# Kernel tuning notes

Hardware: AMD Instinct MI355X
Metric: run time of the kernel (lower is better)

## Reference

```python
import jax, jax.numpy as jnp
import numpy as np

NUM_HEADS = 12
MASK_BIAS = -1000.0


def setup_inputs() -> dict:
    key = jax.random.key(0)
    k1, k2, k3, k4 = jax.random.split(key, 4)
    B, N, C = 2, 2048, 768
    x = jax.random.normal(k1, (B, N, C), dtype=jnp.float32)
    # key-padding mask: 1.0 = masked-out position (gets -1000 bias), 0.0 = visible
    mask = jax.random.randint(k2, (B, N), 0, 2).astype(jnp.float32)
    qkv_w = jax.random.normal(k3, (3 * C, C), dtype=jnp.float32) * (1.0 / np.sqrt(C))
    proj_w = jax.random.normal(k4, (C, C), dtype=jnp.float32) * (1.0 / np.sqrt(C))
    proj_b = jnp.zeros((C,), dtype=jnp.float32)
    return {"x": x, "mask": mask, "qkv_w": qkv_w, "proj_w": proj_w, "proj_b": proj_b}


def reference(x, mask, qkv_w, proj_w, proj_b):
    B, N, C = x.shape
    H = NUM_HEADS
    D = C // H
    scale = D ** (-0.5)
    # qkv: Linear without bias -> [B, N, 3C] -> [3, B, H, N, D]
    qkv = (x @ qkv_w.T).reshape(B, N, 3, H, D).transpose(2, 0, 3, 1, 4)
    q, k, v = qkv[0], qkv[1], qkv[2]
    # scores [B, H, N, N]
    attn = jnp.einsum("bhqd,bhkd->bhqk", q, k) * scale
    attn = attn + mask[:, None, None, :] * MASK_BIAS
    attn = jax.nn.softmax(attn, axis=-1)
    out = jnp.einsum("bhqk,bhkd->bhqd", attn, v)  # [B, H, N, D]
    out = out.transpose(0, 2, 1, 3).reshape(B, N, C)
    return out @ proj_w.T + proj_b
```

## Files before the change

### kernel.cpp

```cpp
#include <hip/hip_runtime.h>

typedef __bf16 bf16_t;
typedef __bf16 bf16x8 __attribute__((ext_vector_type(8)));
typedef float f32x4 __attribute__((ext_vector_type(4)));

#define NUM_B 2
#define NUM_H 12
#define SEQ_N 2048
#define DIM_C 768
#define HEAD_D 64
#define BH_CNT (NUM_B * NUM_H)
#define MTOK (NUM_B * SEQ_N)
#define QSCALE 0.1803368801111137f

#define AS1(p) ((const __attribute__((address_space(1))) void*)(p))
#define AS3(p) ((__attribute__((address_space(3))) void*)(p))

__global__ __launch_bounds__(256) void cvt_scan_kernel(
    const float* __restrict__ s0, const float* __restrict__ s1,
    const float* __restrict__ s2, const float* __restrict__ msk,
    bf16_t* __restrict__ d0, bf16_t* __restrict__ d1, bf16_t* __restrict__ d2,
    int* __restrict__ src, bf16_t* __restrict__ wp, int* __restrict__ cnts,
    int nb0, int nb1, int nb2) {
  __shared__ int psum[256];
  const int blk = blockIdx.x;
  const int t = threadIdx.x;
  if (blk >= nb0 + nb1 + nb2) {
    const int b = blk - (nb0 + nb1 + nb2);
    const float* mb = msk + (size_t)b * SEQ_N;
    int vis[8], c = 0;
#pragma unroll
    for (int j = 0; j < 8; ++j) {
      vis[j] = (mb[t * 8 + j] == 0.0f) ? 1 : 0;
      c += vis[j];
    }
    psum[t] = c;
    __syncthreads();
    for (int off = 1; off < 256; off <<= 1) {
      int v = (t >= off) ? psum[t - off] : 0;
      __syncthreads();
      psum[t] += v;
      __syncthreads();
    }
    const int total = psum[255];
    int vpos = psum[t] - c;
    int mpos = total + (t * 8 - (psum[t] - c));
#pragma unroll
    for (int j = 0; j < 8; ++j) {
      const int tok = t * 8 + j;
      if (vis[j]) {
        src[b * SEQ_N + vpos] = b * SEQ_N + tok;
        wp[b * SEQ_N + vpos] = (bf16_t)1.0f;
        ++vpos;
      } else {
        src[b * SEQ_N + mpos] = b * SEQ_N + tok;
        wp[b * SEQ_N + mpos] = (bf16_t)0.0f;
        ++mpos;
      }
    }
    if (t == 0) {
      cnts[b * 2] = (total + 63) & ~63;
      cnts[b * 2 + 1] = total;
    }
    return;
  }
  const float* sp;
  bf16_t* dp;
  size_t off;
  if (blk < nb0) {
    sp = s0; dp = d0; off = (size_t)blk * 2048;
  } else if (blk < nb0 + nb1) {
    sp = s1; dp = d1; off = (size_t)(blk - nb0) * 2048;
  } else {
    sp = s2; dp = d2; off = (size_t)(blk - nb0 - nb1) * 2048;
  }
  const size_t i = off + (size_t)t * 8;
  float4 f0 = *reinterpret_cast<const float4*>(&sp[i]);
  float4 f1 = *reinterpret_cast<const float4*>(&sp[i + 4]);
  union { ushort4 u; bf16_t h[4]; } p0, p1;
  p0.h[0] = (bf16_t)f0.x; p0.h[1] = (bf16_t)f0.y;
  p0.h[2] = (bf16_t)f0.z; p0.h[3] = (bf16_t)f0.w;
  p1.h[0] = (bf16_t)f1.x; p1.h[1] = (bf16_t)f1.y;
  p1.h[2] = (bf16_t)f1.z; p1.h[3] = (bf16_t)f1.w;
  *reinterpret_cast<ushort4*>(&dp[i]) = p0.u;
  *reinterpret_cast<ushort4*>(&dp[i + 4]) = p1.u;
}

__global__ __launch_bounds__(256, 3) void gemm_qkv_kernel(
    const bf16_t* __restrict__ A, const bf16_t* __restrict__ W,
    const int* __restrict__ src, const int* __restrict__ cnts,
    bf16_t* __restrict__ out) {
  __shared__ __align__(16) bf16_t As[2][128 * 32];
  __shared__ __align__(16) bf16_t Bs[2][128 * 32];

  const int tid = threadIdx.x;
  const int wave = tid >> 6, lane = tid & 63;
  const int quad = lane >> 4, l16 = lane & 15;
  const int m0 = blockIdx.y * 128, n0 = blockIdx.x * 128;
  const int wm = (wave >> 1) * 64, wn = (wave & 1) * 64;
  const bool isQ = (n0 < DIM_C);

  if (!isQ) {
    const int b = m0 >> 11;
    if ((m0 & 2047) >= cnts[b * 2]) return;
  }

  f32x4 acc[4][4] = {};

  const int srow = tid >> 2;
  const int scol = ((tid & 3) ^ ((tid >> 3) & 3)) * 8;
  int ar0, ar1;
  if (isQ) {
    ar0 = m0 + srow;
    ar1 = m0 + srow + 64;
  } else {
    ar0 = src[m0 + srow];
    ar1 = src[m0 + srow + 64];
  }
  const bf16_t* gA0 = A + (size_t)ar0 * DIM_C + scol;
  const bf16_t* gA1 = A + (size_t)ar1 * DIM_C + scol;
  const bf16_t* gB0 = W + (size_t)(n0 + srow) * DIM_C + scol;
  const bf16_t* gB1 = W + (size_t)(n0 + srow + 64) * DIM_C + scol;
  const int lb = wave * 512;

  auto issue = [&](int buf, int k0) {
    __builtin_amdgcn_global_load_lds(AS1(gA0 + k0), AS3(&As[buf][lb]), 16, 0, 0);
    __builtin_amdgcn_global_load_lds(AS1(gA1 + k0), AS3(&As[buf][lb + 2048]), 16, 0, 0);
    __builtin_amdgcn_global_load_lds(AS1(gB0 + k0), AS3(&Bs[buf][lb]), 16, 0, 0);
    __builtin_amdgcn_global_load_lds(AS1(gB1 + k0), AS3(&Bs[buf][lb + 2048]), 16, 0, 0);
  };

  issue(0, 0);
  int cur = 0;
  const int sw = (l16 >> 1) & 3;
  for (int step = 0; step < DIM_C / 32; ++step) {
    __syncthreads();
    if (step + 1 < DIM_C / 32) issue(cur ^ 1, (step + 1) * 32);

    bf16x8 aF[4], bF[4];
#pragma unroll
    for (int mi = 0; mi < 4; ++mi)
      aF[mi] = *reinterpret_cast<const bf16x8*>(
          &As[cur][(wm + mi * 16 + l16) * 32 + ((quad ^ sw) * 8)]);
#pragma unroll
    for (int ni = 0; ni < 4; ++ni)
      bF[ni] = *reinterpret_cast<const bf16x8*>(
          &Bs[cur][(wn + ni * 16 + l16) * 32 + ((quad ^ sw) * 8)]);
#pragma unroll
    for (int mi = 0; mi < 4; ++mi)
#pragma unroll
      for (int ni = 0; ni < 4; ++ni)
        acc[mi][ni] = __builtin_amdgcn_mfma_f32_16x16x32_bf16(aF[mi], bF[ni],
                                                              acc[mi][ni], 0, 0, 0);
    cur ^= 1;
  }

  const size_t per = (size_t)BH_CNT * SEQ_N * HEAD_D;
#pragma unroll
  for (int mi = 0; mi < 4; ++mi) {
#pragma unroll
    for (int ni = 0; ni < 4; ++ni) {
      const int gmB = m0 + wm + mi * 16 + quad * 4;
      const int gn = n0 + wn + ni * 16 + l16;
      const int b = gmB >> 11;
      if (isQ) {
        const int h = gn >> 6, d = gn & 63;
#pragma unroll
        for (int r = 0; r < 4; ++r) {
          const int gm = gmB + r;
          const int tok = gm & 2047;
          out[(((size_t)((gm >> 11) * NUM_H + h) * SEQ_N + tok) * HEAD_D + d)] =
              (bf16_t)(acc[mi][ni][r] * QSCALE);
        }
      } else if (n0 < 2 * DIM_C) {
        const int rem = gn - DIM_C;
        const int h = rem >> 6, d = rem & 63;
#pragma unroll
        for (int r = 0; r < 4; ++r) {
          const int pos = (gmB + r) & 2047;
          out[per + (((size_t)(b * NUM_H + h) * SEQ_N + pos) * HEAD_D + d)] =
              (bf16_t)acc[mi][ni][r];
        }
      } else {
        const int rem = gn - 2 * DIM_C;
        const int h = rem >> 6, d = rem & 63;
        const int pos0 = gmB & 2047;
        const int count = cnts[b * 2 + 1];
        union { ushort4 u; bf16_t h4[4]; } pk;
#pragma unroll
        for (int r = 0; r < 4; ++r)
          pk.h4[r] = (pos0 + r < count) ? (bf16_t)acc[mi][ni][r] : (bf16_t)0.0f;
        *reinterpret_cast<ushort4*>(
            &out[2 * per + (((size_t)(b * NUM_H + h) * HEAD_D + d) * SEQ_N + pos0)]) =
            pk.u;
      }
    }
  }
}

__global__ __launch_bounds__(256, 3) void gemm_proj_kernel(
    const bf16_t* __restrict__ A, const bf16_t* __restrict__ W,
    const float* __restrict__ bias, float* __restrict__ out) {
  __shared__ __align__(16) bf16_t As[2][128 * 32];
  __shared__ __align__(16) bf16_t Bs[2][128 * 32];

  const int tid = threadIdx.x;
  const int wave = tid >> 6, lane = tid & 63;
  const int quad = lane >> 4, l16 = lane & 15;
  const int m0 = blockIdx.y * 128, n0 = blockIdx.x * 128;
  const int wm = (wave >> 1) * 64, wn = (wave & 1) * 64;

  f32x4 acc[4][4] = {};

  const int srow = tid >> 2;
  const int scol = ((tid & 3) ^ ((tid >> 3) & 3)) * 8;
  const bf16_t* gA0 = A + (size_t)(m0 + srow) * DIM_C + scol;
  const bf16_t* gA1 = A + (size_t)(m0 + srow + 64) * DIM_C + scol;
  const bf16_t* gB0 = W + (size_t)(n0 + srow) * DIM_C + scol;
  const bf16_t* gB1 = W + (size_t)(n0 + srow + 64) * DIM_C + scol;
  const int lb = wave * 512;

  auto issue = [&](int buf, int k0) {
    __builtin_amdgcn_global_load_lds(AS1(gA0 + k0), AS3(&As[buf][lb]), 16, 0, 0);
    __builtin_amdgcn_global_load_lds(AS1(gA1 + k0), AS3(&As[buf][lb + 2048]), 16, 0, 0);
    __builtin_amdgcn_global_load_lds(AS1(gB0 + k0), AS3(&Bs[buf][lb]), 16, 0, 0);
    __builtin_amdgcn_global_load_lds(AS1(gB1 + k0), AS3(&Bs[buf][lb + 2048]), 16, 0, 0);
  };

  issue(0, 0);
  int cur = 0;
  const int sw = (l16 >> 1) & 3;
  for (int step = 0; step < DIM_C / 32; ++step) {
    __syncthreads();
    if (step + 1 < DIM_C / 32) issue(cur ^ 1, (step + 1) * 32);

    bf16x8 aF[4], bF[4];
#pragma unroll
    for (int mi = 0; mi < 4; ++mi)
      aF[mi] = *reinterpret_cast<const bf16x8*>(
          &As[cur][(wm + mi * 16 + l16) * 32 + ((quad ^ sw) * 8)]);
#pragma unroll
    for (int ni = 0; ni < 4; ++ni)
      bF[ni] = *reinterpret_cast<const bf16x8*>(
          &Bs[cur][(wn + ni * 16 + l16) * 32 + ((quad ^ sw) * 8)]);
#pragma unroll
    for (int mi = 0; mi < 4; ++mi)
#pragma unroll
      for (int ni = 0; ni < 4; ++ni)
        acc[mi][ni] = __builtin_amdgcn_mfma_f32_16x16x32_bf16(aF[mi], bF[ni],
                                                              acc[mi][ni], 0, 0, 0);
    cur ^= 1;
  }

#pragma unroll
  for (int mi = 0; mi < 4; ++mi) {
#pragma unroll
    for (int ni = 0; ni < 4; ++ni) {
      const int gmB = m0 + wm + mi * 16 + quad * 4;
      const int gn = n0 + wn + ni * 16 + l16;
      const float bv = bias[gn];
#pragma unroll
      for (int r = 0; r < 4; ++r)
        out[(size_t)(gmB + r) * DIM_C + gn] = acc[mi][ni][r] + bv;
    }
  }
}

__global__ __launch_bounds__(256, 3) void attn_kernel(
    const bf16_t* __restrict__ q, const bf16_t* __restrict__ k,
    const bf16_t* __restrict__ vt, const bf16_t* __restrict__ wp,
    const int* __restrict__ cnts, bf16_t* __restrict__ ctx) {
  __shared__ __align__(16) bf16_t Ks[2][128 * 64];
  __shared__ __align__(16) bf16_t Ps[4][1024];

  const int tid = threadIdx.x;
  const int wave = tid >> 6, lane = tid & 63;
  const int quad = lane >> 4, l16 = lane & 15;
  const int bh = blockIdx.y;
  const int b = bh / NUM_H, h = bh - b * NUM_H;
  const int q0 = blockIdx.x * 64 + wave * 16;
  const int cntPad = cnts[b * 2];

  const bf16_t* qb = q + (size_t)bh * SEQ_N * HEAD_D;
  const bf16_t* kb = k + (size_t)bh * SEQ_N * HEAD_D;
  const bf16_t* vtb = vt + (size_t)bh * HEAD_D * SEQ_N;
  const bf16_t* wb = wp + (size_t)b * SEQ_N;

  bf16x8 qf[2];
#pragma unroll
  for (int ks = 0; ks < 2; ++ks)
    qf[ks] = *reinterpret_cast<const bf16x8*>(
        &qb[(size_t)(q0 + l16) * HEAD_D + ks * 32 + quad * 8]);

  f32x4 acc[4] = {};
  f32x4 acc_l = {};

  const int srow = tid >> 3;
  const int scol = ((tid & 7) ^ (srow & 7)) * 8;
  const bf16_t* gK = kb + (size_t)srow * HEAD_D + scol;
  const int lb = wave * 512;

  auto issueK = [&](int buf, int key0) {
#pragma unroll
    for (int p = 0; p < 4; ++p)
      __builtin_amdgcn_global_load_lds(
          AS1(gK + (size_t)(key0 + p * 32) * HEAD_D),
          AS3(&Ks[buf][p * 2048 + lb]), 16, 0, 0);
  };

  issueK(0, 0);
  int cur = 0;
  const int swz = l16 & 7;
  const int psbase = wave * 1024 + l16 * 64;

  for (int key0 = 0; key0 < cntPad; key0 += 128) {
    __syncthreads();
    if (key0 + 128 < cntPad) issueK(cur ^ 1, key0 + 128);

#pragma unroll
    for (int hf = 0; hf < 2; ++hf) {
      const int kbase = key0 + hf * 64;
      if (kbase >= cntPad) break;

      bf16x8 vf[4][2];
#pragma unroll
      for (int dt = 0; dt < 4; ++dt) {
        const bf16_t* vr = &vtb[(size_t)(dt * 16 + l16) * SEQ_N + kbase];
        vf[dt][0] = *reinterpret_cast<const bf16x8*>(&vr[quad * 8]);
        vf[dt][1] = *reinterpret_cast<const bf16x8*>(&vr[32 + quad * 8]);
      }

      f32x4 s[4];
#pragma unroll
      for (int kt = 0; kt < 4; ++kt) {
        const int row = hf * 64 + kt * 16 + l16;
        bf16x8 kf0 = *reinterpret_cast<const bf16x8*>(
            &Ks[cur][row * 64 + ((quad ^ swz) * 8)]);
        bf16x8 kf1 = *reinterpret_cast<const bf16x8*>(
            &Ks[cur][row * 64 + (((4 + quad) ^ swz) * 8)]);
        f32x4 z = {0.0f, 0.0f, 0.0f, 0.0f};
        z = __builtin_amdgcn_mfma_f32_16x16x32_bf16(kf0, qf[0], z, 0, 0, 0);
        s[kt] = __builtin_amdgcn_mfma_f32_16x16x32_bf16(kf1, qf[1], z, 0, 0, 0);
      }

#pragma unroll
      for (int kt = 0; kt < 4; ++kt) {
        union { ushort4 u; bf16_t h4[4]; } pk;
        pk.h4[0] = (bf16_t)exp2f(s[kt][0]);
        pk.h4[1] = (bf16_t)exp2f(s[kt][1]);
        pk.h4[2] = (bf16_t)exp2f(s[kt][2]);
        pk.h4[3] = (bf16_t)exp2f(s[kt][3]);
        const int c = kt * 2 + (quad >> 1);
        *reinterpret_cast<ushort4*>(
            &Ps[0][psbase + ((c ^ swz) << 3) + ((quad & 1) << 2)]) = pk.u;
      }

      bf16x8 pf0 = *reinterpret_cast<const bf16x8*>(
          &Ps[0][psbase + ((quad ^ swz) << 3)]);
      bf16x8 pf1 = *reinterpret_cast<const bf16x8*>(
          &Ps[0][psbase + (((4 + quad) ^ swz) << 3)]);
      bf16x8 wf0 = *reinterpret_cast<const bf16x8*>(&wb[kbase + quad * 8]);
      bf16x8 wf1 = *reinterpret_cast<const bf16x8*>(&wb[kbase + 32 + quad * 8]);
      acc_l = __builtin_amdgcn_mfma_f32_16x16x32_bf16(pf0, wf0, acc_l, 0, 0, 0);
      acc_l = __builtin_amdgcn_mfma_f32_16x16x32_bf16(pf1, wf1, acc_l, 0, 0, 0);

#pragma unroll
      for (int dt = 0; dt < 4; ++dt) {
        acc[dt] =
            __builtin_amdgcn_mfma_f32_16x16x32_bf16(pf0, vf[dt][0], acc[dt], 0, 0, 0);
        acc[dt] =
            __builtin_amdgcn_mfma_f32_16x16x32_bf16(pf1, vf[dt][1], acc[dt], 0, 0, 0);
      }
    }
    cur ^= 1;
  }

  float rl[4];
#pragma unroll
  for (int r = 0; r < 4; ++r) rl[r] = 1.0f / acc_l[r];
#pragma unroll
  for (int dt = 0; dt < 4; ++dt)
#pragma unroll
    for (int r = 0; r < 4; ++r) {
      const int tok = q0 + quad * 4 + r;
      ctx[((size_t)b * SEQ_N + tok) * DIM_C + h * HEAD_D + dt * 16 + l16] =
          (bf16_t)(acc[dt][r] * rl[r]);
    }
}

extern "C" void kernel_launch(void* const* d_in, const int* in_sizes, int n_in,
                              void* d_out, int out_size, void* d_ws,
                              size_t ws_size, hipStream_t stream) {
  const float* x = (const float*)d_in[0];
  const float* mask = (const float*)d_in[1];
  const float* qkv_w = (const float*)d_in[2];
  const float* proj_w = (const float*)d_in[3];
  const float* proj_b = (const float*)d_in[4];
  float* out = (float*)d_out;

  const size_t nx = (size_t)MTOK * DIM_C;
  const size_t nqw = (size_t)3 * DIM_C * DIM_C;
  const size_t npw = (size_t)DIM_C * DIM_C;
  const size_t per = (size_t)BH_CNT * SEQ_N * HEAD_D;

  bf16_t* xb = (bf16_t*)d_ws;
  bf16_t* qwb = xb + nx;
  bf16_t* pwb = qwb + nqw;
  bf16_t* wpb = pwb + npw;
  int* srcb = (int*)(wpb + MTOK);
  int* cntsb = srcb + MTOK;
  bf16_t* qkv = (bf16_t*)(cntsb + 8);
  bf16_t* ctx = qkv + 3 * per;

  const int nb0 = (int)(nx / 2048), nb1 = (int)(nqw / 2048),
            nb2 = (int)(npw / 2048);

  cvt_scan_kernel<<<nb0 + nb1 + nb2 + NUM_B, 256, 0, stream>>>(
      x, qkv_w, proj_w, mask, xb, qwb, pwb, srcb, wpb, cntsb, nb0, nb1, nb2);
  gemm_qkv_kernel<<<dim3(3 * DIM_C / 128, MTOK / 128), 256, 0, stream>>>(
      xb, qwb, srcb, cntsb, qkv);
  attn_kernel<<<dim3(SEQ_N / 64, BH_CNT), 256, 0, stream>>>(
      qkv, qkv + per, qkv + 2 * per, wpb, cntsb, ctx);
  gemm_proj_kernel<<<dim3(DIM_C / 128, MTOK / 128), 256, 0, stream>>>(
      ctx, pwb, proj_b, out);
}
```

Baseline: 175.6 us.

## Store K/V in MFMA fragment layout and split keys across two wave groups

The QKV GEMM epilogue now writes K and V directly in a pre-swizzled MFMA fragment order, so the attention kernel can load operand fragments straight from global memory with contiguous per-lane vector loads instead of staging K through LDS with async copies and barriers. The attention block doubles to 512 threads, with two wave groups each handling half of the visible keys for the same query tile; partial outputs and row sums are merged through shared memory at the end. This removes the per-tile synchronisation and LDS staging and adds parallelism per query tile. In exchange it adds a final reduction step, scattered 2-byte stores in the GEMM epilogue, and more register and LDS use per block.

```diff
diff --git a/kernel.cpp b/kernel.cpp
--- a/kernel.cpp
+++ b/kernel.cpp
@@ -15,6 +15,7 @@
 
 #define AS1(p) ((const __attribute__((address_space(1))) void*)(p))
 #define AS3(p) ((__attribute__((address_space(3))) void*)(p))
+
 
 __global__ __launch_bounds__(256) void cvt_scan_kernel(
     const float* __restrict__ s0, const float* __restrict__ s1,
@@ -174,25 +175,30 @@
         }
       } else if (n0 < 2 * DIM_C) {
         const int rem = gn - DIM_C;
-        const int h = rem >> 6, d = rem & 63;
-#pragma unroll
-        for (int r = 0; r < 4; ++r) {
-          const int pos = (gmB + r) & 2047;
-          out[per + (((size_t)(b * NUM_H + h) * SEQ_N + pos) * HEAD_D + d)] =
-              (bf16_t)acc[mi][ni][r];
-        }
+        const int hh = rem >> 6, d = rem & 63;
+        const int posm = gmB & 2047;
+        const int bh = b * NUM_H + hh;
+        const size_t base = per +
+            (((size_t)(bh * 128 + (posm >> 4)) * 2 + (d >> 5)) * 512 +
+             ((d >> 3) & 3) * 128 + (d & 7));
+        const int l16k = posm & 15;
+#pragma unroll
+        for (int r = 0; r < 4; ++r)
+          out[base + (size_t)(l16k + r) * 8] = (bf16_t)acc[mi][ni][r];
       } else {
         const int rem = gn - 2 * DIM_C;
-        const int h = rem >> 6, d = rem & 63;
-        const int pos0 = gmB & 2047;
+        const int hh = rem >> 6, d = rem & 63;
+        const int posm = gmB & 2047;
+        const int bh = b * NUM_H + hh;
         const int count = cnts[b * 2 + 1];
+        const size_t base = 2 * per +
+            (((size_t)(bh * 64 + (posm >> 5)) * 4 + (d >> 4)) * 512 +
+             ((posm >> 3) & 3) * 128 + (d & 15) * 8 + (posm & 7));
         union { ushort4 u; bf16_t h4[4]; } pk;
 #pragma unroll
         for (int r = 0; r < 4; ++r)
-          pk.h4[r] = (pos0 + r < count) ? (bf16_t)acc[mi][ni][r] : (bf16_t)0.0f;
-        *reinterpret_cast<ushort4*>(
-            &out[2 * per + (((size_t)(b * NUM_H + h) * HEAD_D + d) * SEQ_N + pos0)]) =
-            pk.u;
+          pk.h4[r] = (posm + r < count) ? (bf16_t)acc[mi][ni][r] : (bf16_t)0.0f;
+        *reinterpret_cast<ushort4*>(&out[base]) = pk.u;
       }
     }
   }
@@ -266,24 +272,29 @@
   }
 }
 
-__global__ __launch_bounds__(256, 3) void attn_kernel(
-    const bf16_t* __restrict__ q, const bf16_t* __restrict__ k,
-    const bf16_t* __restrict__ vt, const bf16_t* __restrict__ wp,
+__global__ __launch_bounds__(512, 4) void attn_kernel(
+    const bf16_t* __restrict__ q, const bf16_t* __restrict__ kfr,
+    const bf16_t* __restrict__ vfr, const bf16_t* __restrict__ wp,
     const int* __restrict__ cnts, bf16_t* __restrict__ ctx) {
-  __shared__ __align__(16) bf16_t Ks[2][128 * 64];
-  __shared__ __align__(16) bf16_t Ps[4][1024];
+  __shared__ __align__(16) bf16_t Ps[8][1024];
+  __shared__ float Om[4][16][65];
+  __shared__ float Lm[64];
 
   const int tid = threadIdx.x;
   const int wave = tid >> 6, lane = tid & 63;
   const int quad = lane >> 4, l16 = lane & 15;
+  const int g = wave >> 2, wsub = wave & 3;
   const int bh = blockIdx.y;
   const int b = bh / NUM_H, h = bh - b * NUM_H;
-  const int q0 = blockIdx.x * 64 + wave * 16;
+  const int q0 = blockIdx.x * 64 + wsub * 16;
   const int cntPad = cnts[b * 2];
+  const int half = ((cntPad >> 1) + 63) & ~63;
+  const int kbeg = g ? half : 0;
+  const int kend = g ? cntPad : half;
 
   const bf16_t* qb = q + (size_t)bh * SEQ_N * HEAD_D;
-  const bf16_t* kb = k + (size_t)bh * SEQ_N * HEAD_D;
-  const bf16_t* vtb = vt + (size_t)bh * HEAD_D * SEQ_N;
+  const bf16_t* kbase = kfr + (size_t)bh * 128 * 1024;
+  const bf16_t* vbase = vfr + (size_t)bh * 64 * 2048;
   const bf16_t* wb = wp + (size_t)b * SEQ_N;
 
   bf16x8 qf[2];
@@ -295,97 +306,89 @@
   f32x4 acc[4] = {};
   f32x4 acc_l = {};
 
-  const int srow = tid >> 3;
-  const int scol = ((tid & 7) ^ (srow & 7)) * 8;
-  const bf16_t* gK = kb + (size_t)srow * HEAD_D + scol;
-  const int lb = wave * 512;
-
-  auto issueK = [&](int buf, int key0) {
-#pragma unroll
-    for (int p = 0; p < 4; ++p)
-      __builtin_amdgcn_global_load_lds(
-          AS1(gK + (size_t)(key0 + p * 32) * HEAD_D),
-          AS3(&Ks[buf][p * 2048 + lb]), 16, 0, 0);
-  };
-
-  issueK(0, 0);
-  int cur = 0;
   const int swz = l16 & 7;
   const int psbase = wave * 1024 + l16 * 64;
 
-  for (int key0 = 0; key0 < cntPad; key0 += 128) {
-    __syncthreads();
-    if (key0 + 128 < cntPad) issueK(cur ^ 1, key0 + 128);
-
-#pragma unroll
-    for (int hf = 0; hf < 2; ++hf) {
-      const int kbase = key0 + hf * 64;
-      if (kbase >= cntPad) break;
-
-      bf16x8 vf[4][2];
-#pragma unroll
-      for (int dt = 0; dt < 4; ++dt) {
-        const bf16_t* vr = &vtb[(size_t)(dt * 16 + l16) * SEQ_N + kbase];
-        vf[dt][0] = *reinterpret_cast<const bf16x8*>(&vr[quad * 8]);
-        vf[dt][1] = *reinterpret_cast<const bf16x8*>(&vr[32 + quad * 8]);
+  for (int key0 = kbeg; key0 < kend; key0 += 64) {
+    const bf16_t* kc_p = kbase + (size_t)(key0 >> 4) * 1024 + lane * 8;
+    bf16x8 kf[4][2];
+#pragma unroll
+    for (int kt = 0; kt < 4; ++kt) {
+      kf[kt][0] = *reinterpret_cast<const bf16x8*>(kc_p + kt * 1024);
+      kf[kt][1] = *reinterpret_cast<const bf16x8*>(kc_p + kt * 1024 + 512);
+    }
+    const bf16_t* vc_p = vbase + (size_t)(key0 >> 5) * 2048 + lane * 8;
+    bf16x8 vf[2][4];
+#pragma unroll
+    for (int kc = 0; kc < 2; ++kc)
+#pragma unroll
+      for (int dt = 0; dt < 4; ++dt)
+        vf[kc][dt] = *reinterpret_cast<const bf16x8*>(vc_p + kc * 2048 + dt * 512);
+
+    f32x4 s[4];
+#pragma unroll
+    for (int kt = 0; kt < 4; ++kt) {
+      f32x4 z = {0.0f, 0.0f, 0.0f, 0.0f};
+      z = __builtin_amdgcn_mfma_f32_16x16x32_bf16(kf[kt][0], qf[0], z, 0, 0, 0);
+      s[kt] = __builtin_amdgcn_mfma_f32_16x16x32_bf16(kf[kt][1], qf[1], z, 0, 0, 0);
+    }
+
+#pragma unroll
+    for (int kt = 0; kt < 4; ++kt) {
+      union { ushort4 u; bf16_t h4[4]; } pk;
+      pk.h4[0] = (bf16_t)exp2f(s[kt][0]);
+      pk.h4[1] = (bf16_t)exp2f(s[kt][1]);
+      pk.h4[2] = (bf16_t)exp2f(s[kt][2]);
+      pk.h4[3] = (bf16_t)exp2f(s[kt][3]);
+      const int c = kt * 2 + (quad >> 1);
+      *reinterpret_cast<ushort4*>(
+          &Ps[0][psbase + ((c ^ swz) << 3) + ((quad & 1) << 2)]) = pk.u;
+    }
+
+    bf16x8 pf0 = *reinterpret_cast<const bf16x8*>(
+        &Ps[0][psbase + ((quad ^ swz) << 3)]);
+    bf16x8 pf1 = *reinterpret_cast<const bf16x8*>(
+        &Ps[0][psbase + (((4 + quad) ^ swz) << 3)]);
+    bf16x8 wf0 = *reinterpret_cast<const bf16x8*>(&wb[key0 + quad * 8]);
+    bf16x8 wf1 = *reinterpret_cast<const bf16x8*>(&wb[key0 + 32 + quad * 8]);
+    acc_l = __builtin_amdgcn_mfma_f32_16x16x32_bf16(pf0, wf0, acc_l, 0, 0, 0);
+    acc_l = __builtin_amdgcn_mfma_f32_16x16x32_bf16(pf1, wf1, acc_l, 0, 0, 0);
+
+#pragma unroll
+    for (int dt = 0; dt < 4; ++dt) {
+      acc[dt] = __builtin_amdgcn_mfma_f32_16x16x32_bf16(pf0, vf[0][dt], acc[dt], 0, 0, 0);
+      acc[dt] = __builtin_amdgcn_mfma_f32_16x16x32_bf16(pf1, vf[1][dt], acc[dt], 0, 0, 0);
+    }
+  }
+
+  if (g == 0) {
+#pragma unroll
+    for (int dt = 0; dt < 4; ++dt)
+#pragma unroll
+      for (int r = 0; r < 4; ++r)
+        Om[wsub][quad * 4 + r][dt * 16 + l16] = acc[dt][r];
+    if (l16 == 0) {
+#pragma unroll
+      for (int r = 0; r < 4; ++r) Lm[wsub * 16 + quad * 4 + r] = acc_l[r];
+    }
+  }
+  __syncthreads();
+  if (g == 1) {
+    float rl[4];
+#pragma unroll
+    for (int r = 0; r < 4; ++r)
+      rl[r] = 1.0f / (acc_l[r] + Lm[wsub * 16 + quad * 4 + r]);
+#pragma unroll
+    for (int dt = 0; dt < 4; ++dt)
+#pragma unroll
+      for (int r = 0; r < 4; ++r) {
+        const int tok = q0 + quad * 4 + r;
+        const float val =
+            (acc[dt][r] + Om[wsub][quad * 4 + r][dt * 16 + l16]) * rl[r];
+        ctx[((size_t)b * SEQ_N + tok) * DIM_C + h * HEAD_D + dt * 16 + l16] =
+            (bf16_t)val;
       }
-
-      f32x4 s[4];
-#pragma unroll
-      for (int kt = 0; kt < 4; ++kt) {
-        const int row = hf * 64 + kt * 16 + l16;
-        bf16x8 kf0 = *reinterpret_cast<const bf16x8*>(
-            &Ks[cur][row * 64 + ((quad ^ swz) * 8)]);
-        bf16x8 kf1 = *reinterpret_cast<const bf16x8*>(
-            &Ks[cur][row * 64 + (((4 + quad) ^ swz) * 8)]);
-        f32x4 z = {0.0f, 0.0f, 0.0f, 0.0f};
-        z = __builtin_amdgcn_mfma_f32_16x16x32_bf16(kf0, qf[0], z, 0, 0, 0);
-        s[kt] = __builtin_amdgcn_mfma_f32_16x16x32_bf16(kf1, qf[1], z, 0, 0, 0);
-      }
-
-#pragma unroll
-      for (int kt = 0; kt < 4; ++kt) {
-        union { ushort4 u; bf16_t h4[4]; } pk;
-        pk.h4[0] = (bf16_t)exp2f(s[kt][0]);
-        pk.h4[1] = (bf16_t)exp2f(s[kt][1]);
-        pk.h4[2] = (bf16_t)exp2f(s[kt][2]);
-        pk.h4[3] = (bf16_t)exp2f(s[kt][3]);
-        const int c = kt * 2 + (quad >> 1);
-        *reinterpret_cast<ushort4*>(
-            &Ps[0][psbase + ((c ^ swz) << 3) + ((quad & 1) << 2)]) = pk.u;
-      }
-
-      bf16x8 pf0 = *reinterpret_cast<const bf16x8*>(
-          &Ps[0][psbase + ((quad ^ swz) << 3)]);
-      bf16x8 pf1 = *reinterpret_cast<const bf16x8*>(
-          &Ps[0][psbase + (((4 + quad) ^ swz) << 3)]);
-      bf16x8 wf0 = *reinterpret_cast<const bf16x8*>(&wb[kbase + quad * 8]);
-      bf16x8 wf1 = *reinterpret_cast<const bf16x8*>(&wb[kbase + 32 + quad * 8]);
-      acc_l = __builtin_amdgcn_mfma_f32_16x16x32_bf16(pf0, wf0, acc_l, 0, 0, 0);
-      acc_l = __builtin_amdgcn_mfma_f32_16x16x32_bf16(pf1, wf1, acc_l, 0, 0, 0);
-
-#pragma unroll
-      for (int dt = 0; dt < 4; ++dt) {
-        acc[dt] =
-            __builtin_amdgcn_mfma_f32_16x16x32_bf16(pf0, vf[dt][0], acc[dt], 0, 0, 0);
-        acc[dt] =
-            __builtin_amdgcn_mfma_f32_16x16x32_bf16(pf1, vf[dt][1], acc[dt], 0, 0, 0);
-      }
-    }
-    cur ^= 1;
-  }
-
-  float rl[4];
-#pragma unroll
-  for (int r = 0; r < 4; ++r) rl[r] = 1.0f / acc_l[r];
-#pragma unroll
-  for (int dt = 0; dt < 4; ++dt)
-#pragma unroll
-    for (int r = 0; r < 4; ++r) {
-      const int tok = q0 + quad * 4 + r;
-      ctx[((size_t)b * SEQ_N + tok) * DIM_C + h * HEAD_D + dt * 16 + l16] =
-          (bf16_t)(acc[dt][r] * rl[r]);
-    }
+  }
 }
 
 extern "C" void kernel_launch(void* const* d_in, const int* in_sizes, int n_in,
@@ -419,7 +422,7 @@
       x, qkv_w, proj_w, mask, xb, qwb, pwb, srcb, wpb, cntsb, nb0, nb1, nb2);
   gemm_qkv_kernel<<<dim3(3 * DIM_C / 128, MTOK / 128), 256, 0, stream>>>(
       xb, qwb, srcb, cntsb, qkv);
-  attn_kernel<<<dim3(SEQ_N / 64, BH_CNT), 256, 0, stream>>>(
+  attn_kernel<<<dim3(SEQ_N / 64, BH_CNT), 512, 0, stream>>>(
       qkv, qkv + per, qkv + 2 * per, wpb, cntsb, ctx);
   gemm_proj_kernel<<<dim3(DIM_C / 128, MTOK / 128), 256, 0, stream>>>(
       ctx, pwb, proj_b, out);
```

Result: faster. 157.7 us (-10.2%).
